# Kernel optimization log

Hardware: AMD Instinct MI355X
Metric: run time of the kernel (lower is better)

Reference implementation:

```python
import jax, jax.numpy as jnp
import numpy as np

N_NODES = 100000
N_EDGES = 1600000
IN_DIM = 29
OUT_DIM = 64
BN_EPS = 1e-5


def setup_inputs() -> dict:
    key = jax.random.key(0)
    k1, k2, k3, k4, k5, k6, k7, k8 = jax.random.split(key, 8)
    node = jax.random.normal(k1, (N_NODES, 3), dtype=jnp.float32)
    features = jax.random.normal(k2, (N_NODES, IN_DIM), dtype=jnp.float32)
    edges = jax.random.randint(k3, (N_EDGES, 2), 0, N_NODES, dtype=jnp.int64)
    # Linear(input_dim+3, output_dim, bias=False): weight [out, in+3]
    fan_in = IN_DIM + 3
    weight = jax.random.uniform(k4, (OUT_DIM, fan_in), dtype=jnp.float32,
                                minval=-1.0, maxval=1.0) / np.sqrt(fan_in)
    # BatchNorm1d(output_dim) in eval mode: affine params + running stats
    gamma = jax.random.normal(k5, (OUT_DIM,), dtype=jnp.float32) * 0.1 + 1.0
    beta = jax.random.normal(k6, (OUT_DIM,), dtype=jnp.float32) * 0.1
    running_mean = jax.random.normal(k7, (OUT_DIM,), dtype=jnp.float32) * 0.1
    running_var = jax.random.uniform(k8, (OUT_DIM,), dtype=jnp.float32,
                                     minval=0.5, maxval=1.5)
    return {"node": node, "features": features, "edges": edges,
            "weight": weight, "gamma": gamma, "beta": beta,
            "running_mean": running_mean, "running_var": running_var}


def reference(node, features, edges, weight, gamma, beta, running_mean, running_var):
    dst = edges[:, 0]  # pos_i index (pooling destination)
    src = edges[:, 1]  # pos_j / x_j index
    # gather + concat: msg [E, in+3]
    msg = jnp.concatenate([features[src], node[src] - node[dst]], axis=1)
    # Linear (no bias): [E, out]
    msg = jnp.einsum('ei,oi->eo', msg, weight)
    # BatchNorm1d (eval mode, running stats)
    inv_std = gamma / jnp.sqrt(running_var + BN_EPS)
    msg = (msg - running_mean) * inv_std + beta
    # scatter-max pooling over destination nodes (fixed N segments;
    # torch.unique + scatter_reduce(amax) == segment_max restricted to covered
    # nodes; empty segments filled with 0 matching the zeros init)
    pooled = jax.ops.segment_max(msg, dst, num_segments=N_NODES)
    return jnp.where(jnp.isneginf(pooled), 0.0, pooled)
```

## Files before the change

### kernel.cpp

```cpp
#include <hip/hip_runtime.h>
#include <hip/hip_fp16.h>

#define IN_DIM 29
#define XDIM 32
#define OUT_DIM 64
#define BN_EPS 1e-5f

#define BW      32
#define BW_LOG  5
#define TNODES  64
#define MAXBUCK 4096
#define KCAP    4096
#define SENT    0


__global__ __launch_bounds__(256) void fused_tc_kernel(
    const float* __restrict__ features, const float* __restrict__ node,
    const float* __restrict__ weight, const float* __restrict__ gamma,
    const float* __restrict__ rvar, unsigned short* __restrict__ yq,
    const int* __restrict__ edges, int* __restrict__ gHist,
    int n_nodes, int n_edges, int nbuck, int chunk, int nblk)
{
    __shared__ __align__(16) int smem[MAXBUCK];
    if ((int)blockIdx.x < nblk) {
        int* h = smem;
        for (int i = threadIdx.x; i < nbuck; i += 256) h[i] = 0;
        __syncthreads();
        const int e0 = blockIdx.x * chunk;
        const int e1 = min(e0 + chunk, n_edges);
        const int np = (e1 - e0) >> 1;
        const int4* ep4 = (const int4*)(edges + 2 * e0);
        for (int p = threadIdx.x; p < np; p += 256) {
            int4 v = ep4[p];
            atomicAdd(&h[v.x >> BW_LOG], 1);
            atomicAdd(&h[v.z >> BW_LOG], 1);
        }
        if (((e1 - e0) & 1) && threadIdx.x == 0)
            atomicAdd(&h[edges[2 * (e1 - 1)] >> BW_LOG], 1);
        __syncthreads();
        for (int i = threadIdx.x; i < nbuck; i += 256)
            gHist[i * nblk + blockIdx.x] = h[i];
    } else {
        float* stage = (float*)smem;
        const int tid  = threadIdx.x;
        const int lane = tid & 63, wid = tid >> 6;
        const int n0   = ((int)blockIdx.x - nblk) * TNODES;
        const int nrem = min(TNODES, n_nodes - n0);

        for (int idx = tid; idx < nrem * XDIM; idx += 256) {
            const int r = idx >> 5, c = idx & 31;
            float v = (c < IN_DIM) ? features[(size_t)(n0 + r) * IN_DIM + c]
                                   : node[(size_t)(n0 + r) * 3 + (c - IN_DIM)];
            stage[idx] = v;
        }

        const float a = gamma[lane] * __frsqrt_rn(rvar[lane] + BN_EPS);
        float w[XDIM];
        const float4* wp = (const float4*)(weight + lane * XDIM);
#pragma unroll
        for (int q = 0; q < 8; ++q) {
            float4 v = wp[q];
            w[4*q+0] = v.x * a; w[4*q+1] = v.y * a;
            w[4*q+2] = v.z * a; w[4*q+3] = v.w * a;
        }
        __syncthreads();

        const int r0 = wid * (TNODES / 4);
        const int r1 = min(r0 + TNODES / 4, nrem);
        for (int r = r0; r < r1; ++r) {
            const float4* xs = (const float4*)(stage + r * XDIM);
            float a0 = 0.f, a1 = 0.f, a2 = 0.f, a3 = 0.f;
#pragma unroll
            for (int q = 0; q < 8; ++q) {
                float4 x = xs[q];
                a0 = fmaf(x.x, w[4*q+0], a0);
                a1 = fmaf(x.y, w[4*q+1], a1);
                a2 = fmaf(x.z, w[4*q+2], a2);
                a3 = fmaf(x.w, w[4*q+3], a3);
            }
            const float acc = (a0 + a1) + (a2 + a3);
            unsigned short hh = __half_as_ushort(__float2half(acc));
            unsigned short enc = (hh & 0x8000) ? (unsigned short)(~hh)
                                               : (unsigned short)(hh | 0x8000);
            yq[(size_t)(n0 + r) * OUT_DIM + lane] = enc;
        }
    }
}

__global__ __launch_bounds__(256) void scan_a_kernel(
    int* __restrict__ data, int n, int* __restrict__ aux)
{
    const int t = threadIdx.x;
    const int base = blockIdx.x * 1024 + t * 4;
    int v[4];
#pragma unroll
    for (int k = 0; k < 4; ++k) v[k] = (base + k < n) ? data[base + k] : 0;
    int tsum = v[0] + v[1] + v[2] + v[3];

    const int lane = t & 63, wv = t >> 6;
    int x = tsum;
#pragma unroll
    for (int off = 1; off < 64; off <<= 1) {
        int y = __shfl_up(x, off);
        if (lane >= off) x += y;
    }
    __shared__ int wsum[4];
    if (lane == 63) wsum[wv] = x;
    __syncthreads();
    int wexcl = 0;
    for (int i = 0; i < wv; ++i) wexcl += wsum[i];
    int run = wexcl + x - tsum;
#pragma unroll
    for (int k = 0; k < 4; ++k) {
        if (base + k < n) data[base + k] = run;
        run += v[k];
    }
    if (t == 255) aux[blockIdx.x] = run;
}

__global__ __launch_bounds__(256) void scan_b_kernel(int* __restrict__ aux, int nb) {
    const int t = threadIdx.x;
    const int lane = t & 63, wv = t >> 6;
    __shared__ int wsum[4];
    __shared__ int s_run;
    if (t == 0) s_run = 0;
    __syncthreads();
    for (int base = 0; base < nb; base += 256) {
        const int i = base + t;
        int v = (i < nb) ? aux[i] : 0;
        int x = v;
#pragma unroll
        for (int off = 1; off < 64; off <<= 1) {
            int y = __shfl_up(x, off);
            if (lane >= off) x += y;
        }
        if (lane == 63) wsum[wv] = x;
        __syncthreads();
        int wexcl = 0;
        for (int k = 0; k < wv; ++k) wexcl += wsum[k];
        const int run = s_run;
        if (i < nb) aux[i] = run + wexcl + x - v;
        __syncthreads();
        if (t == 255) s_run = run + wexcl + x;
        __syncthreads();
    }
}

__global__ __launch_bounds__(512) void partition_kernel(
    const int* __restrict__ edges, const int* __restrict__ gOffs,
    const int* __restrict__ aux,
    int* __restrict__ keys, int n_edges, int nbuck, int chunk, int nblk)
{
    __shared__ int cur[MAXBUCK];
    for (int i = threadIdx.x; i < nbuck; i += 512) {
        const int idx = i * nblk + blockIdx.x;
        cur[i] = gOffs[idx] + aux[idx >> 10];
    }
    __syncthreads();
    const int e0 = blockIdx.x * chunk;
    const int e1 = min(e0 + chunk, n_edges);
    const int np = (e1 - e0) >> 1;
    const int4* ep4 = (const int4*)(edges + 2 * e0);
    for (int p = threadIdx.x; p < np; p += 512) {
        int4 v = ep4[p];
        const int b0 = v.x >> BW_LOG;
        const int p0 = atomicAdd(&cur[b0], 1);
        keys[p0] = (v.x & (BW - 1)) | (v.y << BW_LOG);
        const int b1 = v.z >> BW_LOG;
        const int p1 = atomicAdd(&cur[b1], 1);
        keys[p1] = (v.z & (BW - 1)) | (v.w << BW_LOG);
    }
    if (((e1 - e0) & 1) && threadIdx.x == 0) {
        const int dst = edges[2 * (e1 - 1)], src = edges[2 * (e1 - 1) + 1];
        const int b = dst >> BW_LOG;
        const int pos = atomicAdd(&cur[b], 1);
        keys[pos] = (dst & (BW - 1)) | (src << BW_LOG);
    }
}

__global__ __launch_bounds__(512, 4) void pool_fused_kernel(
    const int* __restrict__ gOffs, const int* __restrict__ aux,
    const int* __restrict__ keys,
    const unsigned short* __restrict__ yq, const float* __restrict__ node,
    const float* __restrict__ weight, const float* __restrict__ gamma,
    const float* __restrict__ beta, const float* __restrict__ rmean,
    const float* __restrict__ rvar,
    float* __restrict__ out, int n_nodes, int n_edges, int nbuck, int nblk)
{
    __shared__ int skeys[KCAP];
    __shared__ int hcnt[BW], hoff[BW + 1], hcur[BW];
    const int tid = threadIdx.x;
    const int lane = tid & 63, wid = tid >> 6;
    const int b = blockIdx.x;

    const int i0 = b * nblk;
    const int beg = gOffs[i0] + aux[i0 >> 10];
    int end;
    if (b == nbuck - 1) end = n_edges;
    else {
        const int i1 = (b + 1) * nblk;
        end = gOffs[i1] + aux[i1 >> 10];
    }
    const int cnt = end - beg;

    const float a  = gamma[lane] * __frsqrt_rn(rvar[lane] + BN_EPS);
    const float bp = beta[lane] - rmean[lane] * a;
    const float w29 = weight[lane * XDIM + 29] * a;
    const float w30 = weight[lane * XDIM + 30] * a;
    const float w31 = weight[lane * XDIM + 31] * a;

    if (cnt <= KCAP) {
        if (tid < BW) hcnt[tid] = 0;
        __syncthreads();
        for (int i = tid; i < cnt; i += 512)
            atomicAdd(&hcnt[keys[beg + i] & (BW - 1)], 1);
        __syncthreads();
        if (tid < 64) {
            int v = (lane < BW) ? hcnt[lane] : 0;
            int x = v;
#pragma unroll
            for (int off = 1; off < BW; off <<= 1) {
                int y = __shfl_up(x, off);
                if (lane >= off) x += y;
            }
            if (lane < BW) { hoff[lane] = x - v; hcur[lane] = x - v; }
            if (lane == BW - 1) hoff[BW] = x;
        }
        __syncthreads();
        for (int i = tid; i < cnt; i += 512) {
            const int key = keys[beg + i];
            const int p = atomicAdd(&hcur[key & (BW - 1)], 1);
            skeys[p] = key;
        }
        __syncthreads();

#pragma unroll
        for (int q = 0; q < 4; ++q) {
            const int d = wid + (q << 3);
            const int k0 = hoff[d], k1 = hoff[d + 1];
            unsigned int m = SENT;
            int kk = k0;
            for (; kk + 8 <= k1; kk += 8) {
                unsigned int src[8];
#pragma unroll
                for (int u = 0; u < 8; ++u)
                    src[u] = ((unsigned)skeys[kk + u]) >> BW_LOG;
                unsigned int vv[8];
#pragma unroll
                for (int u = 0; u < 8; ++u)
                    vv[u] = yq[(size_t)src[u] * OUT_DIM + lane];
                __builtin_amdgcn_sched_barrier(0);
#pragma unroll
                for (int u = 0; u < 8; ++u)
                    m = m > vv[u] ? m : vv[u];
            }
            for (; kk < k1; ++kk) {
                const unsigned int s = ((unsigned)skeys[kk]) >> BW_LOG;
                const unsigned int v = yq[(size_t)s * OUT_DIM + lane];
                m = m > v ? m : v;
            }
            const int dg = b * BW + d;
            if (dg < n_nodes) {
                float rr;
                if (m == SENT) {
                    rr = 0.0f;
                } else {
                    const unsigned short enc = (unsigned short)m;
                    const unsigned short h = (enc & 0x8000) ? (unsigned short)(enc ^ 0x8000)
                                                            : (unsigned short)(~enc);
                    const float v = __half2float(__ushort_as_half(h));
                    const float nx = node[(size_t)dg * 3 + 0];
                    const float ny = node[(size_t)dg * 3 + 1];
                    const float nz = node[(size_t)dg * 3 + 2];
                    rr = v + (bp - (w29 * nx + w30 * ny + w31 * nz));
                }
                out[(size_t)dg * OUT_DIM + lane] = rr;
            }
        }
    } else {
        int* acc = skeys;
        for (int i = tid; i < BW * OUT_DIM; i += 512) acc[i] = SENT;
        __syncthreads();
        for (int i = beg + wid; i < end; i += 8) {
            const int key = keys[i];
            const int d = key & (BW - 1);
            const unsigned int v = yq[(size_t)((unsigned)key >> BW_LOG) * OUT_DIM + lane];
            atomicMax(&acc[d * OUT_DIM + lane], (int)v);
        }
        __syncthreads();
        for (int d = wid; d < BW; d += 8) {
            const int dg = b * BW + d;
            if (dg >= n_nodes) break;
            const int k = acc[d * OUT_DIM + lane];
            float rr;
            if (k == SENT) {
                rr = 0.0f;
            } else {
                const unsigned short enc = (unsigned short)k;
                const unsigned short h = (enc & 0x8000) ? (unsigned short)(enc ^ 0x8000)
                                                        : (unsigned short)(~enc);
                const float v = __half2float(__ushort_as_half(h));
                const float nx = node[(size_t)dg * 3 + 0];
                const float ny = node[(size_t)dg * 3 + 1];
                const float nz = node[(size_t)dg * 3 + 2];
                rr = v + (bp - (w29 * nx + w30 * ny + w31 * nz));
            }
            out[(size_t)dg * OUT_DIM + lane] = rr;
        }
    }
}

__global__ void init_kernel(int4* __restrict__ out, int total4) {
    int t = blockIdx.x * blockDim.x + threadIdx.x;
    if (t < total4) out[t] = make_int4(INT_MIN, INT_MIN, INT_MIN, INT_MIN);
}

__global__ __launch_bounds__(256) void edge_atomic_kernel(
    const int* __restrict__ edges,
    const float* __restrict__ features, const float* __restrict__ node,
    const float* __restrict__ weight, const float* __restrict__ gamma,
    const float* __restrict__ beta, const float* __restrict__ rmean,
    const float* __restrict__ rvar,
    int* __restrict__ out, int n_edges, int epw)
{
    const int lane = threadIdx.x & 63;
    const int wave = (blockIdx.x * blockDim.x + threadIdx.x) >> 6;
    int e0 = wave * epw, e1 = e0 + epw;
    if (e1 > n_edges) e1 = n_edges;

    float w[XDIM];
    const float4* wp = (const float4*)(weight + lane * XDIM);
#pragma unroll
    for (int q = 0; q < 8; ++q) {
        float4 v = wp[q];
        w[4*q+0] = v.x; w[4*q+1] = v.y; w[4*q+2] = v.z; w[4*q+3] = v.w;
    }
    const float a = gamma[lane] * __frsqrt_rn(rvar[lane] + BN_EPS);
    const float bprime = beta[lane] - rmean[lane] * a;

    for (int e = e0; e < e1; ++e) {
        const int dst = edges[2*e+0], src = edges[2*e+1];
        float x[XDIM];
#pragma unroll
        for (int i = 0; i < IN_DIM; ++i) x[i] = features[(size_t)src * IN_DIM + i];
#pragma unroll
        for (int j = 0; j < 3; ++j)
            x[IN_DIM+j] = node[(size_t)src*3+j] - node[(size_t)dst*3+j];
        float acc = 0.0f;
#pragma unroll
        for (int i = 0; i < XDIM; ++i) acc = fmaf(x[i], w[i], acc);
        float msg = fmaf(acc, a, bprime);
        int bb = __float_as_int(msg);
        int key = (bb < 0) ? (bb ^ 0x7FFFFFFF) : bb;
        atomicMax(out + (size_t)dst * OUT_DIM + lane, key);
    }
}

__global__ void decode_kernel(int* __restrict__ out, int total) {
    int t = blockIdx.x * blockDim.x + threadIdx.x;
    if (t >= total) return;
    int k = out[t];
    float r;
    if (k == INT_MIN) r = 0.0f;
    else { int b = (k < 0) ? (k ^ 0x7FFFFFFF) : k; r = __int_as_float(b); }
    ((float*)out)[t] = r;
}

extern "C" void kernel_launch(void* const* d_in, const int* in_sizes, int n_in,
                              void* d_out, int out_size, void* d_ws, size_t ws_size,
                              hipStream_t stream) {
    const float* node     = (const float*)d_in[0];
    const float* features = (const float*)d_in[1];
    const int*   edges    = (const int*)d_in[2];
    const float* weight   = (const float*)d_in[3];
    const float* gamma    = (const float*)d_in[4];
    const float* beta     = (const float*)d_in[5];
    const float* rmean    = (const float*)d_in[6];
    const float* rvar     = (const float*)d_in[7];

    const int n_nodes = in_sizes[0] / 3;
    const int n_edges = in_sizes[2] / 2;

    const int nbuck = (n_nodes + BW - 1) >> BW_LOG;

    int nblk = 0; size_t o_yq=0, o_hist=0, o_aux=0, o_keys=0; size_t need = 0;
    for (int cand = 256; cand >= 32; cand >>= 1) {
        const int n_scan = nbuck * cand;
        const int nb_scan = (n_scan + 1023) / 1024;
        size_t off = 0;
        auto alloc = [&](size_t bytes) { size_t r = off; off = (off + bytes + 15) & ~(size_t)15; return r; };
        o_yq   = alloc((size_t)n_nodes * OUT_DIM * sizeof(unsigned short));
        o_hist = alloc((size_t)n_scan * sizeof(int));
        o_aux  = alloc((size_t)nb_scan * sizeof(int));
        o_keys = alloc((size_t)n_edges * sizeof(int));
        need = off;
        if (need <= ws_size) { nblk = cand; break; }
    }

    if (nblk > 0 && nbuck <= MAXBUCK && n_nodes <= MAXBUCK * BW) {
        const int n_scan = nbuck * nblk;
        const int nb_scan = (n_scan + 1023) / 1024;
        int chunk = (n_edges + nblk - 1) / nblk;
        chunk = (chunk + 1) & ~1;
        const int ntb = (n_nodes + TNODES - 1) / TNODES;

        char* base  = (char*)d_ws;
        unsigned short* yq = (unsigned short*)(base + o_yq);
        int* gHist  = (int*)(base + o_hist);
        int* aux    = (int*)(base + o_aux);
        int* keys   = (int*)(base + o_keys);

        fused_tc_kernel<<<nblk + ntb, 256, 0, stream>>>(
            features, node, weight, gamma, rvar, yq,
            edges, gHist, n_nodes, n_edges, nbuck, chunk, nblk);
        scan_a_kernel<<<nb_scan, 256, 0, stream>>>(gHist, n_scan, aux);
        scan_b_kernel<<<1, 256, 0, stream>>>(aux, nb_scan);
        partition_kernel<<<nblk, 512, 0, stream>>>(edges, gHist, aux, keys,
                                                   n_edges, nbuck, chunk, nblk);
        pool_fused_kernel<<<nbuck, 512, 0, stream>>>(
            gHist, aux, keys, yq, node, weight, gamma, beta, rmean, rvar,
            (float*)d_out, n_nodes, n_edges, nbuck, nblk);
    } else {
        int* out_i = (int*)d_out;
        const int total4 = out_size / 4;
        init_kernel<<<(total4 + 255) / 256, 256, 0, stream>>>((int4*)out_i, total4);
        const int n_waves = 8192;
        const int epw = (n_edges + n_waves - 1) / n_waves;
        edge_atomic_kernel<<<n_waves / 4, 256, 0, stream>>>(
            edges, features, node, weight, gamma, beta, rmean, rvar,
            out_i, n_edges, epw);
        decode_kernel<<<(out_size + 255) / 256, 256, 0, stream>>>(out_i, out_size);
    }
}
```

Baseline: 191.5 us.

## Store histogram block-major and scan per-bucket columns before a bucket-base scan

The per-block bucket histogram is now stored row-major by block, so writes in the histogram and partition kernels are coalesced. A new column-scan kernel gives each thread one bucket, computes exclusive prefixes across blocks in place and emits per-bucket totals. The existing single-block scan then turns those totals into bucket base offsets. The pool kernel reads its bucket range directly from the base array instead of combining two arrays. The column scan is serial over blocks per thread and launches only a few blocks (about 13 for ~3125 buckets), trading the parallel flat scan for lower parallelism.

```diff
diff --git a/kernel.cpp b/kernel.cpp
--- a/kernel.cpp
+++ b/kernel.cpp
@@ -18,7 +18,7 @@
     const float* __restrict__ features, const float* __restrict__ node,
     const float* __restrict__ weight, const float* __restrict__ gamma,
     const float* __restrict__ rvar, unsigned short* __restrict__ yq,
-    const int* __restrict__ edges, int* __restrict__ gHist,
+    const int* __restrict__ edges, int* __restrict__ H,
     int n_nodes, int n_edges, int nbuck, int chunk, int nblk)
 {
     __shared__ __align__(16) int smem[MAXBUCK];
@@ -38,8 +38,9 @@
         if (((e1 - e0) & 1) && threadIdx.x == 0)
             atomicAdd(&h[edges[2 * (e1 - 1)] >> BW_LOG], 1);
         __syncthreads();
+        int* hrow = H + (size_t)blockIdx.x * nbuck;
         for (int i = threadIdx.x; i < nbuck; i += 256)
-            gHist[i * nblk + blockIdx.x] = h[i];
+            hrow[i] = h[i];
     } else {
         float* stage = (float*)smem;
         const int tid  = threadIdx.x;
@@ -87,35 +88,20 @@
     }
 }
 
-__global__ __launch_bounds__(256) void scan_a_kernel(
-    int* __restrict__ data, int n, int* __restrict__ aux)
+__global__ __launch_bounds__(256) void scan_t_kernel(
+    int* __restrict__ H, int* __restrict__ colsum, int nbuck, int nblk)
 {
-    const int t = threadIdx.x;
-    const int base = blockIdx.x * 1024 + t * 4;
-    int v[4];
-#pragma unroll
-    for (int k = 0; k < 4; ++k) v[k] = (base + k < n) ? data[base + k] : 0;
-    int tsum = v[0] + v[1] + v[2] + v[3];
-
-    const int lane = t & 63, wv = t >> 6;
-    int x = tsum;
-#pragma unroll
-    for (int off = 1; off < 64; off <<= 1) {
-        int y = __shfl_up(x, off);
-        if (lane >= off) x += y;
-    }
-    __shared__ int wsum[4];
-    if (lane == 63) wsum[wv] = x;
-    __syncthreads();
-    int wexcl = 0;
-    for (int i = 0; i < wv; ++i) wexcl += wsum[i];
-    int run = wexcl + x - tsum;
-#pragma unroll
-    for (int k = 0; k < 4; ++k) {
-        if (base + k < n) data[base + k] = run;
-        run += v[k];
-    }
-    if (t == 255) aux[blockIdx.x] = run;
+    const int b = blockIdx.x * 256 + threadIdx.x;
+    if (b >= nbuck) return;
+    int run = 0;
+#pragma unroll 4
+    for (int k = 0; k < nblk; ++k) {
+        const size_t idx = (size_t)k * nbuck + b;
+        const int v = H[idx];
+        H[idx] = run;
+        run += v;
+    }
+    colsum[b] = run;
 }
 
 __global__ __launch_bounds__(256) void scan_b_kernel(int* __restrict__ aux, int nb) {
@@ -147,15 +133,14 @@
 }
 
 __global__ __launch_bounds__(512) void partition_kernel(
-    const int* __restrict__ edges, const int* __restrict__ gOffs,
-    const int* __restrict__ aux,
+    const int* __restrict__ edges, const int* __restrict__ H,
+    const int* __restrict__ base,
     int* __restrict__ keys, int n_edges, int nbuck, int chunk, int nblk)
 {
     __shared__ int cur[MAXBUCK];
-    for (int i = threadIdx.x; i < nbuck; i += 512) {
-        const int idx = i * nblk + blockIdx.x;
-        cur[i] = gOffs[idx] + aux[idx >> 10];
-    }
+    const int* hrow = H + (size_t)blockIdx.x * nbuck;
+    for (int i = threadIdx.x; i < nbuck; i += 512)
+        cur[i] = base[i] + hrow[i];
     __syncthreads();
     const int e0 = blockIdx.x * chunk;
     const int e1 = min(e0 + chunk, n_edges);
@@ -179,13 +164,12 @@
 }
 
 __global__ __launch_bounds__(512, 4) void pool_fused_kernel(
-    const int* __restrict__ gOffs, const int* __restrict__ aux,
-    const int* __restrict__ keys,
+    const int* __restrict__ base, const int* __restrict__ keys,
     const unsigned short* __restrict__ yq, const float* __restrict__ node,
     const float* __restrict__ weight, const float* __restrict__ gamma,
     const float* __restrict__ beta, const float* __restrict__ rmean,
     const float* __restrict__ rvar,
-    float* __restrict__ out, int n_nodes, int n_edges, int nbuck, int nblk)
+    float* __restrict__ out, int n_nodes, int n_edges, int nbuck)
 {
     __shared__ int skeys[KCAP];
     __shared__ int hcnt[BW], hoff[BW + 1], hcur[BW];
@@ -193,14 +177,8 @@
     const int lane = tid & 63, wid = tid >> 6;
     const int b = blockIdx.x;
 
-    const int i0 = b * nblk;
-    const int beg = gOffs[i0] + aux[i0 >> 10];
-    int end;
-    if (b == nbuck - 1) end = n_edges;
-    else {
-        const int i1 = (b + 1) * nblk;
-        end = gOffs[i1] + aux[i1 >> 10];
-    }
+    const int beg = base[b];
+    const int end = (b == nbuck - 1) ? n_edges : base[b + 1];
     const int cnt = end - beg;
 
     const float a  = gamma[lane] * __frsqrt_rn(rvar[lane] + BN_EPS);
@@ -383,43 +361,39 @@
 
     const int nbuck = (n_nodes + BW - 1) >> BW_LOG;
 
-    int nblk = 0; size_t o_yq=0, o_hist=0, o_aux=0, o_keys=0; size_t need = 0;
+    int nblk = 0; size_t o_yq=0, o_hist=0, o_base=0, o_keys=0; size_t need = 0;
     for (int cand = 256; cand >= 32; cand >>= 1) {
-        const int n_scan = nbuck * cand;
-        const int nb_scan = (n_scan + 1023) / 1024;
         size_t off = 0;
         auto alloc = [&](size_t bytes) { size_t r = off; off = (off + bytes + 15) & ~(size_t)15; return r; };
         o_yq   = alloc((size_t)n_nodes * OUT_DIM * sizeof(unsigned short));
-        o_hist = alloc((size_t)n_scan * sizeof(int));
-        o_aux  = alloc((size_t)nb_scan * sizeof(int));
+        o_hist = alloc((size_t)nbuck * cand * sizeof(int));
+        o_base = alloc((size_t)nbuck * sizeof(int));
         o_keys = alloc((size_t)n_edges * sizeof(int));
         need = off;
         if (need <= ws_size) { nblk = cand; break; }
     }
 
     if (nblk > 0 && nbuck <= MAXBUCK && n_nodes <= MAXBUCK * BW) {
-        const int n_scan = nbuck * nblk;
-        const int nb_scan = (n_scan + 1023) / 1024;
         int chunk = (n_edges + nblk - 1) / nblk;
         chunk = (chunk + 1) & ~1;
         const int ntb = (n_nodes + TNODES - 1) / TNODES;
 
-        char* base  = (char*)d_ws;
-        unsigned short* yq = (unsigned short*)(base + o_yq);
-        int* gHist  = (int*)(base + o_hist);
-        int* aux    = (int*)(base + o_aux);
-        int* keys   = (int*)(base + o_keys);
+        char* baseptr  = (char*)d_ws;
+        unsigned short* yq = (unsigned short*)(baseptr + o_yq);
+        int* H      = (int*)(baseptr + o_hist);
+        int* bucketBase = (int*)(baseptr + o_base);
+        int* keys   = (int*)(baseptr + o_keys);
 
         fused_tc_kernel<<<nblk + ntb, 256, 0, stream>>>(
             features, node, weight, gamma, rvar, yq,
-            edges, gHist, n_nodes, n_edges, nbuck, chunk, nblk);
-        scan_a_kernel<<<nb_scan, 256, 0, stream>>>(gHist, n_scan, aux);
-        scan_b_kernel<<<1, 256, 0, stream>>>(aux, nb_scan);
-        partition_kernel<<<nblk, 512, 0, stream>>>(edges, gHist, aux, keys,
+            edges, H, n_nodes, n_edges, nbuck, chunk, nblk);
+        scan_t_kernel<<<(nbuck + 255) / 256, 256, 0, stream>>>(H, bucketBase, nbuck, nblk);
+        scan_b_kernel<<<1, 256, 0, stream>>>(bucketBase, nbuck);
+        partition_kernel<<<nblk, 512, 0, stream>>>(edges, H, bucketBase, keys,
                                                    n_edges, nbuck, chunk, nblk);
         pool_fused_kernel<<<nbuck, 512, 0, stream>>>(
-            gHist, aux, keys, yq, node, weight, gamma, beta, rmean, rvar,
-            (float*)d_out, n_nodes, n_edges, nbuck, nblk);
+            bucketBase, keys, yq, node, weight, gamma, beta, rmean, rvar,
+            (float*)d_out, n_nodes, n_edges, nbuck);
     } else {
         int* out_i = (int*)d_out;
         const int total4 = out_size / 4;
```

Result: slower. 227.5 us (+18.8%).
